# Performance work log

Hardware: AMD Instinct MI355X
Metric: run time of the kernel (lower is better)

Reference implementation:

```python
import jax, jax.numpy as jnp
from jax import lax
import numpy as np

ACTBIT = 8
B, CIN, COUT, H, W, K = 32, 16, 16, 256, 256, 3


def setup_inputs() -> dict:
    key = jax.random.key(0)
    k1, k2, k3, k4 = jax.random.split(key, 4)
    x = jax.random.normal(k1, (B, CIN, H, W), dtype=jnp.float32)
    # quantized int8 weight values stored as float (already deadzone-quantized + descaled ints)
    weight_int8 = jnp.round(jnp.clip(jax.random.normal(k2, (COUT, CIN, K, K)) * 40.0, -127.0, 127.0)).astype(jnp.float32)
    # per-output-channel power-of-two weight scale: 2**delta, delta in [-8, -4)
    delta = jax.random.randint(k3, (COUT,), -8, -4).astype(jnp.float32)
    scale_weight = jnp.exp2(delta).astype(jnp.float32)
    bias = jax.random.normal(k4, (COUT,), dtype=jnp.float32)
    return {"x": x, "weight_int8": weight_int8, "scale_weight": scale_weight, "bias": bias}


def reference(x, weight_int8, scale_weight, bias):
    n = 2.0 ** (ACTBIT - 1) - 1.0  # 127
    # channel-last, as in tochannellast
    x_cl = jnp.transpose(x, (0, 2, 3, 1))  # [B,H,W,Cin]
    # dynamic activation scale: max|x| / 2^(actbit-1)
    scale_input = jnp.max(jnp.abs(x_cl)) / (2.0 ** (ACTBIT - 1))
    # fast_qfn: div, clamp to [-n, n], round  (integer-valued activations)
    x_q = jnp.round(jnp.clip(x_cl / scale_input, -n, n))
    # int conv (emulated in fp32 on integer-valued tensors), stride 1, pad 1
    w_hwio = jnp.transpose(weight_int8, (2, 3, 1, 0))  # [K,K,Cin,Cout]
    acc = lax.conv_general_dilated(
        x_q, w_hwio, window_strides=(1, 1), padding=((1, 1), (1, 1)),
        dimension_numbers=("NHWC", "HWIO", "NHWC"))  # [B,H,W,Cout]
    # dequant: scalar input scale * per-output-channel weight scale, then bias
    out = acc * (scale_input * scale_weight) + bias
    # back to channel-first
    return jnp.transpose(out, (0, 3, 1, 2))
```

## Files before the change

kernel.cpp:

```cpp
#include <hip/hip_runtime.h>
#include <hip/hip_bf16.h>

#define B_    32
#define H_    256
#define W_    256
#define ROWS  8
#define LR    (ROWS + 2)
#define LCP   68
#define RSTR  (LCP*2)
#define BUFU  (LR*RSTR)
#define NT    8
#define NTILES (B_*(H_/ROWS)*(W_/64))

typedef float f32x4 __attribute__((ext_vector_type(4)));
typedef short s16x8 __attribute__((ext_vector_type(8)));

__device__ inline unsigned short f2bf(float f){
  __hip_bfloat16 h = __float2bfloat16(f);
  return __builtin_bit_cast(unsigned short, h);
}

__device__ inline float quant1(float v, float rinv, float s, float hs){
  float q0 = rintf(v * rinv);
  float d  = fmaf(q0, -s, v);
  q0 += (d >  hs) ? 1.f : 0.f;
  q0 -= (d < -hs) ? 1.f : 0.f;
  return fminf(fmaxf(q0, -127.f), 127.f);
}

__device__ __forceinline__ void tile_decode(int t, int& b, int& w0, int& h0){
  int hg = t & 31; int r = t >> 5;
  w0 = (r & 3) * 64; b = r >> 2; h0 = hg * ROWS;
}

__device__ __forceinline__ void build_packA(const float* __restrict__ wq,
                                            unsigned short* __restrict__ packA,
                                            int l){
  int co = l & 15;
  int g  = l >> 4;
  for (int mm2 = 0; mm2 < 5; ++mm2){
    for (int i = 0; i < 8; ++i){
      int kappa = g*8 + i;
      int tap = 2*mm2 + (kappa >> 4);
      int ci  = kappa & 15;
      float v = (tap <= 8) ? wq[(co*16 + ci)*9 + tap] : 0.f;
      packA[(mm2*64 + l)*8 + i] = f2bf(v);
    }
  }
}

__global__ __launch_bounds__(256) void absmax_kernel(const float* __restrict__ x,
                                                     const float* __restrict__ wq,
                                                     float* __restrict__ pmax,
                                                     unsigned short* __restrict__ packA,
                                                     int n4){
  __shared__ float red[4];
  int idx = blockIdx.x*blockDim.x + threadIdx.x;
  int stride = gridDim.x*blockDim.x;
  float m = 0.f;
  for (int i = idx; i < n4; i += stride){
    float4 v = reinterpret_cast<const float4*>(x)[i];
    m = fmaxf(m, fmaxf(fmaxf(fabsf(v.x), fabsf(v.y)), fmaxf(fabsf(v.z), fabsf(v.w))));
  }
  #pragma unroll
  for (int off = 32; off > 0; off >>= 1)
    m = fmaxf(m, __shfl_xor(m, off));
  int lane = threadIdx.x & 63, wid = threadIdx.x >> 6;
  if (lane == 0) red[wid] = m;
  __syncthreads();
  if (threadIdx.x == 0)
    pmax[blockIdx.x] = fmaxf(fmaxf(red[0], red[1]), fmaxf(red[2], red[3]));
  if (blockIdx.x == 0 && threadIdx.x < 64) build_packA(wq, packA, threadIdx.x);
}

template<int NGRP, int RBASE>
__device__ __forceinline__ void q_load_t(const float* __restrict__ x,
                                         int b, int w0, int h0,
                                         int tid, int lane, int wid,
                                         float v[][8], float tv[8]){
  const int KMAX  = (NGRP + 7) / 8;
  const int NTAIL = (NGRP / 2) * 4;
  const int c = lane;
  const int win = w0 - 1 + c;
  const bool colok = (unsigned)win < 256u;
  #pragma unroll
  for (int k = 0; k < KMAX; ++k){
    int gi = wid + 8*k;
    bool act = gi < NGRP;
    int r = RBASE + (gi >> 1), half = gi & 1;
    int hin = h0 + r - 1;
    bool rowok = (unsigned)hin < 256u;
    bool ok = act && rowok && colok;
    const float* p = x + ((size_t)(b*16 + half*8) << 16) + (size_t)(rowok ? hin : 0)*256 + win;
    #pragma unroll
    for (int ci = 0; ci < 8; ++ci)
      v[k][ci] = ok ? p[(size_t)ci << 16] : 0.f;
  }
  if (tid >= 448 && tid < 448 + NTAIL){
    int t = tid - 448;
    int t_c = 64 + (t & 1), t_half = (t >> 1) & 1, t_r = RBASE + (t >> 2);
    int hin = h0 + t_r - 1;
    bool rowok = (unsigned)hin < 256u;
    int twin = w0 - 1 + t_c;
    bool ok = rowok && ((unsigned)twin < 256u);
    const float* p = x + ((size_t)(b*16 + t_half*8) << 16) + (size_t)(rowok ? hin : 0)*256 + twin;
    #pragma unroll
    for (int ci = 0; ci < 8; ++ci)
      tv[ci] = ok ? p[(size_t)ci << 16] : 0.f;
  }
}

template<int NGRP, int RBASE>
__device__ __forceinline__ void q_write_t(s16x8* ldsv, int bufoff,
                                          int tid, int lane, int wid,
                                          const float v[][8], const float tv[8],
                                          float rinv, float s, float hs){
  const int KMAX  = (NGRP + 7) / 8;
  const int NTAIL = (NGRP / 2) * 4;
  const int c = lane;
  #pragma unroll
  for (int k = 0; k < KMAX; ++k){
    int gi = wid + 8*k;
    if (gi < NGRP){
      int r = RBASE + (gi >> 1), half = gi & 1;
      s16x8 qv;
      #pragma unroll
      for (int ci = 0; ci < 8; ++ci)
        qv[ci] = (short)f2bf(quant1(v[k][ci], rinv, s, hs));
      int u = (r*RSTR + c*2 + half) ^ ((c >> 2) & 7);
      ldsv[bufoff + u] = qv;
    }
  }
  if (tid >= 448 && tid < 448 + NTAIL){
    int t = tid - 448;
    int t_c = 64 + (t & 1), t_half = (t >> 1) & 1, t_r = RBASE + (t >> 2);
    s16x8 qv;
    #pragma unroll
    for (int ci = 0; ci < 8; ++ci)
      qv[ci] = (short)f2bf(quant1(tv[ci], rinv, s, hs));
    int u = (t_r*RSTR + t_c*2 + t_half) ^ ((t_c >> 2) & 7);
    ldsv[bufoff + u] = qv;
  }
}

__device__ __forceinline__ void c_phase(const s16x8* ldsv, int bufoff,
                                        const s16x8 A[5], const int kr[5], const int kw[5],
                                        int lane, int wid, int b, int w0, int h0,
                                        const float sc[4], const float bb[4],
                                        float* __restrict__ out){
  const int colg = lane & 15;
  const int g    = lane >> 4;
  const int hlf  = g & 1;
  f32x4 acc[4] = {};
  #pragma unroll
  for (int n = 0; n < 4; ++n){
    #pragma unroll
    for (int m = 0; m < 5; ++m){
      int cc = n*16 + colg + kw[m];
      int u = ((wid + kr[m])*RSTR + cc*2 + hlf) ^ ((cc >> 2) & 7);
      acc[n] = __builtin_amdgcn_mfma_f32_16x16x32_bf16(A[m], ldsv[bufoff + u], acc[n], 0, 0, 0);
    }
  }
  const int h = h0 + wid;
  #pragma unroll
  for (int j = 0; j < 4; ++j){
    const int co = g*4 + j;
    float* op = out + ((size_t)(b*16 + co) << 16) + h*256 + w0 + colg;
    #pragma unroll
    for (int n = 0; n < 4; ++n)
      __builtin_nontemporal_store(acc[n][j] * sc[j] + bb[j], op + n*16);
  }
}

__global__ __launch_bounds__(512)
void fconv_kernel(const float* __restrict__ x,
                  const float* __restrict__ sw,
                  const float* __restrict__ bias,
                  const float* __restrict__ pmax,
                  const unsigned short* __restrict__ packA,
                  float* __restrict__ out){
  __shared__ __align__(16) unsigned short lds[2*LR*LCP*16];
  __shared__ float redmax[8];
  s16x8* ldsv = reinterpret_cast<s16x8*>(lds);

  const int tid  = threadIdx.x;
  const int lane = tid & 63;
  const int wid  = tid >> 6;

  const int bid = blockIdx.x;
  const int t0  = (bid & 7)*512 + (bid >> 3)*NT;

  int b, w0, h0;
  float v[3][8], tv[8];

  tile_decode(t0, b, w0, h0);
  q_load_t<20,0>(x, b, w0, h0, tid, lane, wid, v, tv);

  float4 pv = reinterpret_cast<const float4*>(pmax)[tid];
  float m = fmaxf(fmaxf(pv.x, pv.y), fmaxf(pv.z, pv.w));
  #pragma unroll
  for (int off = 32; off > 0; off >>= 1)
    m = fmaxf(m, __shfl_xor(m, off));
  if (lane == 0) redmax[wid] = m;
  __syncthreads();
  float gm = redmax[0];
  #pragma unroll
  for (int i = 1; i < 8; ++i) gm = fmaxf(gm, redmax[i]);

  const float s    = gm * 0.0078125f;
  const float rinv = 1.0f / s;
  const float hs   = 0.5f * s;

  const int g   = lane >> 4;
  const int tlg = g >> 1;
  int kr[5], kw[5];
  #pragma unroll
  for (int mm = 0; mm < 5; ++mm){
    int t = 2*mm + tlg; if (t > 8) t = 8;
    kr[mm] = (t*11) >> 5;
    kw[mm] = t - kr[mm]*3;
  }
  s16x8 A[5];
  const s16x8* pA = reinterpret_cast<const s16x8*>(packA);
  #pragma unroll
  for (int mm = 0; mm < 5; ++mm) A[mm] = pA[mm*64 + lane];
  float sc[4], bb[4];
  #pragma unroll
  for (int j = 0; j < 4; ++j){
    sc[j] = s * sw[g*4 + j];
    bb[j] = bias[g*4 + j];
  }

  q_write_t<20,0>(ldsv, 0, tid, lane, wid, v, tv, rinv, s, hs);
  __syncthreads();

  #pragma unroll
  for (int k = 0; k < NT; ++k){
    const int cur = k & 1;
    if (k < NT-1){
      int b2, w2, h2; tile_decode(t0 + k + 1, b2, w2, h2);
      q_load_t<16,2>(x, b2, w2, h2, tid, lane, wid, v, tv);
      if (tid < 2*RSTR){
        int rr = tid >= RSTR;
        int cc = tid - rr*RSTR;
        ldsv[(cur^1)*BUFU + rr*RSTR + cc] = ldsv[cur*BUFU + (8+rr)*RSTR + cc];
      }
    }
    tile_decode(t0 + k, b, w0, h0);
    c_phase(ldsv, cur*BUFU, A, kr, kw, lane, wid, b, w0, h0, sc, bb, out);
    if (k < NT-1)
      q_write_t<16,2>(ldsv, (cur^1)*BUFU, tid, lane, wid, v, tv, rinv, s, hs);
    __syncthreads();
  }
}

extern "C" void kernel_launch(void* const* d_in, const int* in_sizes, int n_in,
                              void* d_out, int out_size, void* d_ws, size_t ws_size,
                              hipStream_t stream){
  const float* x    = (const float*)d_in[0];
  const float* wq   = (const float*)d_in[1];
  const float* sw   = (const float*)d_in[2];
  const float* bias = (const float*)d_in[3];
  float* out = (float*)d_out;
  unsigned short* packA = (unsigned short*)((char*)d_ws + 64);
  float* pmax = (float*)((char*)d_ws + 8192);

  absmax_kernel<<<2048, 256, 0, stream>>>(x, wq, pmax, packA, (B_*16*H_*W_)/4);
  fconv_kernel<<<NTILES/NT, 512, 0, stream>>>(x, sw, bias, pmax, packA, out);
}
```

Before: 82.64 us.

## Prefetch next tile via async global-to-LDS loads instead of registers

Replaces the register-held prefetch of the next tile's input rows with `__builtin_amdgcn_global_load_lds` DMA into a raw fp32 LDS staging buffer. After the MFMA compute phase, the staged values are read back from LDS, quantized to bf16 and written into the swizzled tile buffer. The aim is to free the vector registers that held prefetched data and let loads proceed asynchronously during compute. In exchange it adds roughly 33 KB of LDS per block, a second barrier per iteration and extra LDS traffic, and drops the full unroll of the tile loop. These costs could reduce occupancy or add latency.

```diff
diff --git a/kernel.cpp b/kernel.cpp
--- a/kernel.cpp
+++ b/kernel.cpp
@@ -11,9 +11,12 @@
 #define BUFU  (LR*RSTR)
 #define NT    8
 #define NTILES (B_*(H_/ROWS)*(W_/64))
+#define RAWB  (128*64)
+#define RAWH  256
 
 typedef float f32x4 __attribute__((ext_vector_type(4)));
 typedef short s16x8 __attribute__((ext_vector_type(8)));
+typedef unsigned int u32;
 
 __device__ inline unsigned short f2bf(float f){
   __hip_bfloat16 h = __float2bfloat16(f);
@@ -73,21 +76,18 @@
   if (blockIdx.x == 0 && threadIdx.x < 64) build_packA(wq, packA, threadIdx.x);
 }
 
-template<int NGRP, int RBASE>
-__device__ __forceinline__ void q_load_t(const float* __restrict__ x,
-                                         int b, int w0, int h0,
-                                         int tid, int lane, int wid,
-                                         float v[][8], float tv[8]){
-  const int KMAX  = (NGRP + 7) / 8;
-  const int NTAIL = (NGRP / 2) * 4;
+__device__ __forceinline__ void q_load_full(const float* __restrict__ x,
+                                            int b, int w0, int h0,
+                                            int tid, int lane, int wid,
+                                            float v[3][8], float tv[8]){
   const int c = lane;
   const int win = w0 - 1 + c;
   const bool colok = (unsigned)win < 256u;
   #pragma unroll
-  for (int k = 0; k < KMAX; ++k){
+  for (int k = 0; k < 3; ++k){
     int gi = wid + 8*k;
-    bool act = gi < NGRP;
-    int r = RBASE + (gi >> 1), half = gi & 1;
+    bool act = gi < 20;
+    int r = gi >> 1, half = gi & 1;
     int hin = h0 + r - 1;
     bool rowok = (unsigned)hin < 256u;
     bool ok = act && rowok && colok;
@@ -96,9 +96,9 @@
     for (int ci = 0; ci < 8; ++ci)
       v[k][ci] = ok ? p[(size_t)ci << 16] : 0.f;
   }
-  if (tid >= 448 && tid < 448 + NTAIL){
+  if (tid >= 448 && tid < 488){
     int t = tid - 448;
-    int t_c = 64 + (t & 1), t_half = (t >> 1) & 1, t_r = RBASE + (t >> 2);
+    int t_c = 64 + (t & 1), t_half = (t >> 1) & 1, t_r = t >> 2;
     int hin = h0 + t_r - 1;
     bool rowok = (unsigned)hin < 256u;
     int twin = w0 - 1 + t_c;
@@ -110,37 +110,90 @@
   }
 }
 
-template<int NGRP, int RBASE>
-__device__ __forceinline__ void q_write_t(s16x8* ldsv, int bufoff,
-                                          int tid, int lane, int wid,
-                                          const float v[][8], const float tv[8],
-                                          float rinv, float s, float hs){
-  const int KMAX  = (NGRP + 7) / 8;
-  const int NTAIL = (NGRP / 2) * 4;
+__device__ __forceinline__ void q_write_full(s16x8* ldsv,
+                                             int tid, int lane, int wid,
+                                             const float v[3][8], const float tv[8],
+                                             float rinv, float s, float hs){
   const int c = lane;
   #pragma unroll
-  for (int k = 0; k < KMAX; ++k){
+  for (int k = 0; k < 3; ++k){
     int gi = wid + 8*k;
-    if (gi < NGRP){
-      int r = RBASE + (gi >> 1), half = gi & 1;
+    if (gi < 20){
+      int r = gi >> 1, half = gi & 1;
       s16x8 qv;
       #pragma unroll
       for (int ci = 0; ci < 8; ++ci)
         qv[ci] = (short)f2bf(quant1(v[k][ci], rinv, s, hs));
       int u = (r*RSTR + c*2 + half) ^ ((c >> 2) & 7);
-      ldsv[bufoff + u] = qv;
-    }
-  }
-  if (tid >= 448 && tid < 448 + NTAIL){
+      ldsv[u] = qv;
+    }
+  }
+  if (tid >= 448 && tid < 488){
     int t = tid - 448;
-    int t_c = 64 + (t & 1), t_half = (t >> 1) & 1, t_r = RBASE + (t >> 2);
+    int t_c = 64 + (t & 1), t_half = (t >> 1) & 1, t_r = t >> 2;
     s16x8 qv;
     #pragma unroll
     for (int ci = 0; ci < 8; ++ci)
       qv[ci] = (short)f2bf(quant1(tv[ci], rinv, s, hs));
     int u = (t_r*RSTR + t_c*2 + t_half) ^ ((t_c >> 2) & 7);
-    ldsv[bufoff + u] = qv;
-  }
+    ldsv[u] = qv;
+  }
+}
+
+__device__ __forceinline__ void dma_stage(const float* __restrict__ x,
+                                          int b, int w0, int h02,
+                                          int lane, int wid, u32* raw){
+  int hin2 = h02 + wid + 1;
+  int hinc = hin2 > 255 ? 255 : hin2;
+  #pragma unroll
+  for (int ci = 0; ci < 16; ++ci){
+    const float* g = x + ((size_t)(b*16 + ci) << 16) + (size_t)hinc*256 + (w0 + lane);
+    __builtin_amdgcn_global_load_lds(
+        (const __attribute__((address_space(1))) u32*)g,
+        (__attribute__((address_space(3))) u32*)(raw + (wid*16 + ci)*64), 4, 0, 0);
+  }
+  if (wid < 4){
+    int e = wid*64 + lane;
+    int p = e >> 1, side = e & 1;
+    int rr = p >> 4, ci = p & 15;
+    int hh = h02 + rr + 1; hh = hh > 255 ? 255 : hh;
+    int win2 = side ? (w0 + 64) : (w0 - 1);
+    win2 = win2 < 0 ? 0 : (win2 > 255 ? 255 : win2);
+    const float* g = x + ((size_t)(b*16 + ci) << 16) + (size_t)hh*256 + win2;
+    __builtin_amdgcn_global_load_lds(
+        (const __attribute__((address_space(1))) u32*)g,
+        (__attribute__((address_space(3))) u32*)(raw + RAWB + wid*64), 4, 0, 0);
+  }
+}
+
+__device__ __forceinline__ void quant_pair(s16x8* ldsq, int bufoff, const u32* raw,
+                                           int rr, int c, int half, bool rowok, int w0,
+                                           float rinv, float s, float hs){
+  bool ok = rowok && (c == 0 ? (w0 > 0) : (c == 65 ? (w0 < 192) : true));
+  s16x8 qv;
+  #pragma unroll
+  for (int i = 0; i < 8; ++i){
+    int ci = half*8 + i;
+    int p  = rr*16 + ci;
+    u32 bits = (c >= 1 && c <= 64) ? raw[p*64 + (c - 1)]
+                                   : raw[RAWB + p*2 + (c != 0)];
+    float val = ok ? __uint_as_float(bits) : 0.f;
+    qv[i] = (short)f2bf(quant1(val, rinv, s, hs));
+  }
+  int r = rr + 2;
+  int u = (r*RSTR + c*2 + half) ^ ((c >> 2) & 7);
+  ldsq[bufoff + u] = qv;
+}
+
+__device__ __forceinline__ void quant_from_raw(s16x8* ldsq, int bufoff, const u32* raw,
+                                               int lane, int wid, int w0, int h02,
+                                               float rinv, float s, float hs){
+  const int rr = wid;
+  const bool rowok = (h02 + rr + 1) < 256;
+  quant_pair(ldsq, bufoff, raw, rr, lane, 0, rowok, w0, rinv, s, hs);
+  quant_pair(ldsq, bufoff, raw, rr, lane, 1, rowok, w0, rinv, s, hs);
+  if (lane < 4)
+    quant_pair(ldsq, bufoff, raw, rr, 64 + (lane >> 1), lane & 1, rowok, w0, rinv, s, hs);
 }
 
 __device__ __forceinline__ void c_phase(const s16x8* ldsv, int bufoff,
@@ -179,9 +232,10 @@
                   const float* __restrict__ pmax,
                   const unsigned short* __restrict__ packA,
                   float* __restrict__ out){
-  __shared__ __align__(16) unsigned short lds[2*LR*LCP*16];
+  __shared__ __align__(16) unsigned short lds_q[2*LR*LCP*16];
+  __shared__ __align__(16) u32 lds_raw[RAWB + RAWH];
   __shared__ float redmax[8];
-  s16x8* ldsv = reinterpret_cast<s16x8*>(lds);
+  s16x8* ldsq = reinterpret_cast<s16x8*>(lds_q);
 
   const int tid  = threadIdx.x;
   const int lane = tid & 63;
@@ -194,7 +248,7 @@
   float v[3][8], tv[8];
 
   tile_decode(t0, b, w0, h0);
-  q_load_t<20,0>(x, b, w0, h0, tid, lane, wid, v, tv);
+  q_load_full(x, b, w0, h0, tid, lane, wid, v, tv);
 
   float4 pv = reinterpret_cast<const float4*>(pmax)[tid];
   float m = fmaxf(fmaxf(pv.x, pv.y), fmaxf(pv.z, pv.w));
@@ -231,26 +285,28 @@
     bb[j] = bias[g*4 + j];
   }
 
-  q_write_t<20,0>(ldsv, 0, tid, lane, wid, v, tv, rinv, s, hs);
+  q_write_full(ldsq, tid, lane, wid, v, tv, rinv, s, hs);
   __syncthreads();
 
-  #pragma unroll
   for (int k = 0; k < NT; ++k){
     const int cur = k & 1;
     if (k < NT-1){
       int b2, w2, h2; tile_decode(t0 + k + 1, b2, w2, h2);
-      q_load_t<16,2>(x, b2, w2, h2, tid, lane, wid, v, tv);
+      dma_stage(x, b2, w2, h2, lane, wid, lds_raw);
+    }
+    tile_decode(t0 + k, b, w0, h0);
+    c_phase(ldsq, cur*BUFU, A, kr, kw, lane, wid, b, w0, h0, sc, bb, out);
+    if (k < NT-1){
+      __syncthreads();
       if (tid < 2*RSTR){
-        int rr = tid >= RSTR;
-        int cc = tid - rr*RSTR;
-        ldsv[(cur^1)*BUFU + rr*RSTR + cc] = ldsv[cur*BUFU + (8+rr)*RSTR + cc];
+        int rr2 = tid >= RSTR;
+        int cc2 = tid - rr2*RSTR;
+        ldsq[(cur^1)*BUFU + rr2*RSTR + cc2] = ldsq[cur*BUFU + (8+rr2)*RSTR + cc2];
       }
-    }
-    tile_decode(t0 + k, b, w0, h0);
-    c_phase(ldsv, cur*BUFU, A, kr, kw, lane, wid, b, w0, h0, sc, bb, out);
-    if (k < NT-1)
-      q_write_t<16,2>(ldsv, (cur^1)*BUFU, tid, lane, wid, v, tv, rinv, s, hs);
-    __syncthreads();
+      int b2, w2, h2; tile_decode(t0 + k + 1, b2, w2, h2);
+      quant_from_raw(ldsq, (cur^1)*BUFU, lds_raw, lane, wid, w2, h2, rinv, s, hs);
+      __syncthreads();
+    }
   }
 }
 
```

Measured after the change: 82.65 us. Within noise of the previous version (+0.0%).
